# Performance work log

Measured on AMD Instinct MI355X. Metric: run time of the kernel, lower is better.

The kernel has to match this reference:

```python
import jax, jax.numpy as jnp
import numpy as np

N = 100000
E = 3200000
IN_DIM = 500
HID = 64
OUT_DIM = 40
K = 10
ALPHA = 0.1
BN_EPS = 1e-5


def setup_inputs() -> dict:
    key = jax.random.key(0)
    ks = jax.random.split(key, 10)
    x = jax.random.normal(ks[0], (N, IN_DIM), dtype=jnp.float32)
    edge_index = jax.random.randint(ks[1], (2, E), 0, N, dtype=jnp.int64)
    W1 = jax.random.normal(ks[2], (IN_DIM, HID), dtype=jnp.float32) / np.sqrt(IN_DIM)
    b1 = jnp.zeros((HID,), dtype=jnp.float32)
    bn_gamma = jnp.ones((HID,), dtype=jnp.float32)
    bn_beta = jnp.zeros((HID,), dtype=jnp.float32)
    bn_mean = jax.random.normal(ks[3], (HID,), dtype=jnp.float32) * 0.1
    bn_var = jax.random.uniform(ks[4], (HID,), dtype=jnp.float32) + 0.5
    W2 = jax.random.normal(ks[5], (HID, OUT_DIM), dtype=jnp.float32) / np.sqrt(HID)
    b2 = jnp.zeros((OUT_DIM,), dtype=jnp.float32)
    return {"x": x, "edge_index": edge_index, "W1": W1, "b1": b1,
            "bn_gamma": bn_gamma, "bn_beta": bn_beta, "bn_mean": bn_mean,
            "bn_var": bn_var, "W2": W2, "b2": b2}


def _gcn_norm(edge_index):
    # PyG gcn_norm with add_self_loops=True, symmetric normalization.
    row = jnp.concatenate([edge_index[0], jnp.arange(N, dtype=edge_index.dtype)])
    col = jnp.concatenate([edge_index[1], jnp.arange(N, dtype=edge_index.dtype)])
    deg = jax.ops.segment_sum(jnp.ones_like(col, dtype=jnp.float32), col, num_segments=N)
    dinv = jnp.where(deg > 0, jax.lax.rsqrt(deg), 0.0)
    norm = dinv[row] * dinv[col]  # [E+N]
    return row, col, norm


def _appnp(x, row, col, norm):
    h = x
    def step(xk, _):
        msg = norm[:, None] * xk[row]                       # [E+N, HID] gather
        agg = jax.ops.segment_sum(msg, col, num_segments=N)  # scatter-add
        return (1.0 - ALPHA) * agg + ALPHA * h, None
    xK, _ = jax.lax.scan(step, x, None, length=K)
    return xK


def reference(x, edge_index, W1, b1, bn_gamma, bn_beta, bn_mean, bn_var, W2, b2):
    row, col, norm = _gcn_norm(edge_index)
    h = x @ W1 + b1                                   # lin1
    h = _appnp(h, row, col, norm)                     # K-step APPNP
    h = (h - bn_mean) * jax.lax.rsqrt(bn_var + BN_EPS) * bn_gamma + bn_beta  # BN (eval)
    # dropout is identity in eval mode
    emb = h @ W2 + b2                                 # lin2
    out = jax.nn.log_softmax(emb, axis=1)
    return out, emb
```

## Files before the change

### kernel.cpp

```cpp
#include <hip/hip_runtime.h>
#include <math.h>

#define N_NODES 100000
#define N_EDGES 3200000
#define IN_DIM  500
#define HID     64
#define OUT_DIM 40
#define K_ITERS 10
#define ALPHA   0.1f
#define BN_EPS  1e-5f

#define WPAD 48
#define YD   40
#define YH   20
#define NBUCK 782
#define TILE_A 8192
#define APG 48
#define NQ 8
#define QSHIFT 14

__device__ __forceinline__ void unpack8(uint4 v, float f[8]) {
    f[0] = __uint_as_float(v.x << 16);
    f[1] = __uint_as_float(v.x & 0xffff0000u);
    f[2] = __uint_as_float(v.y << 16);
    f[3] = __uint_as_float(v.y & 0xffff0000u);
    f[4] = __uint_as_float(v.z << 16);
    f[5] = __uint_as_float(v.z & 0xffff0000u);
    f[6] = __uint_as_float(v.w << 16);
    f[7] = __uint_as_float(v.w & 0xffff0000u);
}
__device__ __forceinline__ unsigned pack2(float a, float b) {
    unsigned ua = __float_as_uint(a);
    unsigned ub = __float_as_uint(b);
    ua += ((ua >> 16) & 1u) + 0x7fffu;
    ub += ((ub >> 16) & 1u) + 0x7fffu;
    return (ua >> 16) | (ub & 0xffff0000u);
}
__device__ __forceinline__ float edge_w(unsigned e) {
    return __uint_as_float((e >> 17) << 16);
}
__device__ __forceinline__ void fma8(float acc[8], float wgt, const float f[8]) {
#pragma unroll
    for (int i = 0; i < 8; ++i) acc[i] = fmaf(wgt, f[i], acc[i]);
}


__global__ void zero_cnt_kernel(int* __restrict__ cntq) {
    int i = blockIdx.x * 256 + threadIdx.x;
    if (i < NQ * N_NODES) cntq[i] = 0;
}

__global__ void hist_kernel(const int* __restrict__ ei, int* __restrict__ cntq) {
    int e = blockIdx.x * 256 + threadIdx.x;
    if (e < N_EDGES) {
        int r = ei[e];
        int c = ei[N_EDGES + e];
        atomicAdd(&cntq[(r >> QSHIFT) * N_NODES + c], 1);
    }
}

__global__ void reduce_kernel(const int* __restrict__ cntq, int* __restrict__ psum) {
    __shared__ int s[256];
    int i = blockIdx.x * 256 + threadIdx.x;
    int v = 0;
    if (i < N_NODES) {
#pragma unroll
        for (int q = 0; q < NQ; ++q) v += cntq[q * N_NODES + i];
    }
    s[threadIdx.x] = v;
    __syncthreads();
    for (int off = 128; off > 0; off >>= 1) {
        if (threadIdx.x < (unsigned)off) s[threadIdx.x] += s[threadIdx.x + off];
        __syncthreads();
    }
    if (threadIdx.x == 0) psum[blockIdx.x] = s[0];
}

__global__ void scanp_kernel(const int* __restrict__ psum, int* __restrict__ pexcl,
                             int nparts) {
    __shared__ int s[512];
    int t = threadIdx.x;
    int v = (t < nparts) ? psum[t] : 0;
    s[t] = v;
    __syncthreads();
    for (int off = 1; off < 512; off <<= 1) {
        int tv = (t >= off) ? s[t - off] : 0;
        __syncthreads();
        s[t] += tv;
        __syncthreads();
    }
    if (t < nparts) pexcl[t] = s[t] - v;
}

__global__ void apply_kernel(const int* __restrict__ cntq, const int* __restrict__ pexcl,
                             int* __restrict__ rowptr, float* __restrict__ dinv) {
    __shared__ int s[256];
    int t = threadIdx.x;
    int i = blockIdx.x * 256 + t;
    int v = 0;
    if (i < N_NODES) {
#pragma unroll
        for (int q = 0; q < NQ; ++q) v += cntq[q * N_NODES + i];
    }
    s[t] = v;
    __syncthreads();
    for (int off = 1; off < 256; off <<= 1) {
        int tv = (t >= off) ? s[t - off] : 0;
        __syncthreads();
        s[t] += tv;
        __syncthreads();
    }
    if (i < N_NODES) {
        int excl = pexcl[blockIdx.x] + s[t] - v;
        rowptr[i] = excl;
        dinv[i] = rsqrtf((float)(v + 1));
        if (i == N_NODES - 1) rowptr[N_NODES] = excl + v;
    }
}


__global__ void bcur_init_kernel(const int* __restrict__ rowptr, int* __restrict__ bcursor) {
    int i = blockIdx.x * 256 + threadIdx.x;
    if (i < NBUCK) bcursor[i] = rowptr[i << 7];
}

__global__ __launch_bounds__(256) void bucketA_kernel(const int* __restrict__ ei,
                                                      int* __restrict__ bcursor,
                                                      unsigned* __restrict__ ebuf) {
    __shared__ int cnt[NBUCK];
    __shared__ int gbase[NBUCK];
    for (int i = threadIdx.x; i < NBUCK; i += 256) cnt[i] = 0;
    __syncthreads();
    const int e0 = blockIdx.x * TILE_A;
    const int e1 = (e0 + TILE_A < N_EDGES) ? e0 + TILE_A : N_EDGES;
    for (int e = e0 + threadIdx.x; e < e1; e += 256)
        atomicAdd(&cnt[ei[N_EDGES + e] >> 7], 1);
    __syncthreads();
    for (int i = threadIdx.x; i < NBUCK; i += 256) {
        int n = cnt[i];
        gbase[i] = (n > 0) ? atomicAdd(&bcursor[i], n) : 0;
        cnt[i] = 0;
    }
    __syncthreads();
    for (int e = e0 + threadIdx.x; e < e1; e += 256) {
        int r = ei[e];
        int c = ei[N_EDGES + e];
        int b = c >> 7;
        int rank = atomicAdd(&cnt[b], 1);
        ebuf[gbase[b] + rank] = (unsigned)r | ((unsigned)(c & 127) << 17);
    }
}

__global__ __launch_bounds__(256) void bucketB_kernel(const unsigned* __restrict__ ebuf,
                                                      const int* __restrict__ rowptr,
                                                      const int* __restrict__ cntq,
                                                      const float* __restrict__ dinv,
                                                      unsigned* __restrict__ ew) {
    __shared__ int lcur[NQ * 128];
    __shared__ float ldinv[128];
    const int base = blockIdx.x << 7;
    const int nn = (N_NODES - base < 128) ? (N_NODES - base) : 128;
    if (threadIdx.x < (unsigned)nn) {
        const int gi = base + threadIdx.x;
        int run = rowptr[gi];
#pragma unroll
        for (int q = 0; q < NQ; ++q) {
            lcur[q * 128 + threadIdx.x] = run;
            run += cntq[q * N_NODES + gi];
        }
        ldinv[threadIdx.x] = dinv[gi];
    }
    __syncthreads();
    const int s0 = rowptr[base];
    const int hi = (base + 128 < N_NODES) ? base + 128 : N_NODES;
    const int s1 = rowptr[hi];
    for (int p = s0 + threadIdx.x; p < s1; p += 256) {
        unsigned v = ebuf[p];
        int r = v & 0x1ffff;
        int cl = v >> 17;
        int q = r >> QSHIFT;
        int pos = atomicAdd(&lcur[q * 128 + cl], 1);
        float w = dinv[r] * ldinv[cl];
        unsigned f = __float_as_uint(w) + 0x8000u;
        ew[pos] = (unsigned)r | ((f >> 16) << 17);
    }
}

__global__ void prep_kernel(const float* __restrict__ W2, const float* __restrict__ gamma,
                            const float* __restrict__ beta, const float* __restrict__ mean,
                            const float* __restrict__ var, const float* __restrict__ b1,
                            const float* __restrict__ b2, float* __restrict__ W2p,
                            float* __restrict__ c1, float* __restrict__ cbeta) {
    __shared__ float sc[64];
    __shared__ float sd[64];
    int t = threadIdx.x;
    if (t < 64) {
        float s = rsqrtf(var[t] + BN_EPS) * gamma[t];
        sc[t] = s;
        sd[t] = beta[t] - mean[t] * s;
    }
    __syncthreads();
    for (int i = t; i < 64 * OUT_DIM; i += 256) {
        int f = i / OUT_DIM;
        W2p[i] = sc[f] * W2[i];
    }
    if (t < WPAD) {
        if (t < OUT_DIM) {
            float acb = b2[t], ac1 = 0.f;
            for (int f = 0; f < 64; ++f) {
                float w2 = W2[f * OUT_DIM + t];
                acb = fmaf(sd[f], w2, acb);
                ac1 = fmaf(b1[f] * sc[f], w2, ac1);
            }
            cbeta[t] = acb;
            c1[t] = ac1;
        } else {
            c1[t] = 0.f;
        }
    }
}

__global__ __launch_bounds__(256) void wc_kernel(const float* __restrict__ W1,
                                                 const float* __restrict__ W2p,
                                                 float* __restrict__ Wc) {
    __shared__ float w2s[64 * OUT_DIM];
    for (int i = threadIdx.x; i < 64 * OUT_DIM; i += 256) w2s[i] = W2p[i];
    __syncthreads();
    int idx = blockIdx.x * 256 + threadIdx.x;
    if (idx >= IN_DIM * WPAD) return;
    int k = idx / WPAD, o = idx % WPAD;
    float a = 0.f;
    if (o < OUT_DIM) {
        const float* w1r = W1 + (size_t)k * HID;
#pragma unroll 8
        for (int f = 0; f < 64; ++f) a = fmaf(w1r[f], w2s[f * OUT_DIM + o], a);
    }
    Wc[idx] = a;
}

#define L1_M  128
#define L1_KC 20
#define L1_PITCH 132
__global__ __launch_bounds__(256) void lin1_kernel(const float* __restrict__ x,
                                                   const float* __restrict__ Wc,
                                                   const float* __restrict__ c1,
                                                   float* __restrict__ y0f,
                                                   unsigned* __restrict__ y0b) {
    __shared__ float xsT[L1_KC * L1_PITCH];
    __shared__ float wcs[L1_KC * WPAD];

    const int t = threadIdx.x;
    const int ng = t & 31;
    const int og = t >> 5;
    const int nbase = blockIdx.x * L1_M;

    const int srow = t >> 1;
    const int skb  = (t & 1) * 10;
    const int gsrc = nbase + srow;
    const int gcl  = (gsrc < N_NODES) ? gsrc : (N_NODES - 1);
    const float* xrow = x + (size_t)gcl * IN_DIM;

    float acc[4][6];
#pragma unroll
    for (int i = 0; i < 4; ++i)
#pragma unroll
        for (int j = 0; j < 6; ++j) acc[i][j] = 0.0f;

    float2 xr[5];
    float wr[4];
#pragma unroll
    for (int u = 0; u < 5; ++u) xr[u] = *(const float2*)(xrow + skb + 2 * u);
#pragma unroll
    for (int j = 0; j < 4; ++j) {
        int i = t + j * 256;
        if (i < L1_KC * WPAD) wr[j] = Wc[i];
    }

    for (int k0 = 0; k0 < IN_DIM; k0 += L1_KC) {
#pragma unroll
        for (int u = 0; u < 5; ++u) {
            xsT[(skb + 2 * u) * L1_PITCH + srow]     = xr[u].x;
            xsT[(skb + 2 * u + 1) * L1_PITCH + srow] = xr[u].y;
        }
#pragma unroll
        for (int j = 0; j < 4; ++j) {
            int i = t + j * 256;
            if (i < L1_KC * WPAD) wcs[i] = wr[j];
        }
        __syncthreads();

        const int kn = k0 + L1_KC;
        if (kn < IN_DIM) {
#pragma unroll
            for (int u = 0; u < 5; ++u) xr[u] = *(const float2*)(xrow + kn + skb + 2 * u);
#pragma unroll
            for (int j = 0; j < 4; ++j) {
                int i = t + j * 256;
                if (i < L1_KC * WPAD) wr[j] = Wc[(size_t)kn * WPAD + i];
            }
        }

#pragma unroll 4
        for (int k = 0; k < L1_KC; ++k) {
            const float4 xv = *(const float4*)&xsT[k * L1_PITCH + ng * 4];
            float w[6];
#pragma unroll
            for (int j = 0; j < 6; ++j) w[j] = wcs[k * WPAD + og * 6 + j];
            const float xr4[4] = {xv.x, xv.y, xv.z, xv.w};
#pragma unroll
            for (int i = 0; i < 4; ++i)
#pragma unroll
                for (int j = 0; j < 6; ++j)
                    acc[i][j] = fmaf(xr4[i], w[j], acc[i][j]);
        }
        __syncthreads();
    }

    float cc[6];
#pragma unroll
    for (int j = 0; j < 6; ++j) cc[j] = c1[og * 6 + j];
#pragma unroll
    for (int i = 0; i < 4; ++i) {
        const int n = nbase + ng * 4 + i;
        if (n < N_NODES) {
            float o[6];
#pragma unroll
            for (int j = 0; j < 6; ++j) o[j] = acc[i][j] + cc[j];
            float* yf = y0f + (size_t)n * YD + og * 6;
            unsigned* yb = y0b + (size_t)n * YH + og * 3;
            if (og < 6) {
                *(float2*)(yf)     = make_float2(o[0], o[1]);
                *(float2*)(yf + 2) = make_float2(o[2], o[3]);
                *(float2*)(yf + 4) = make_float2(o[4], o[5]);
                yb[0] = pack2(o[0], o[1]);
                yb[1] = pack2(o[2], o[3]);
                yb[2] = pack2(o[4], o[5]);
            } else if (og == 6) {
                *(float2*)(yf)     = make_float2(o[0], o[1]);
                *(float2*)(yf + 2) = make_float2(o[2], o[3]);
                yb[0] = pack2(o[0], o[1]);
                yb[1] = pack2(o[2], o[3]);
            }
        }
    }
}

template <bool LAST>
__global__ __launch_bounds__(256) void appnp40_kernel(const int* __restrict__ rowptr,
                                                      const unsigned* __restrict__ ew,
                                                      const float* __restrict__ dinv,
                                                      const unsigned* __restrict__ yin,
                                                      const float* __restrict__ h,
                                                      unsigned* __restrict__ yout,
                                                      float* __restrict__ yKf) {
    const int wv   = threadIdx.x >> 6;
    const int lane = threadIdx.x & 63;
    const int sub  = lane / 5;
    const int dl   = lane - sub * 5;
    const int node = blockIdx.x * APG + wv * 12 + sub;
    const bool act = (lane < 60) && (node < N_NODES);
    const int dl4  = dl * 4;

    int beg = 0, end = 0;
    float selfw = 0.f;
    if (act) {
        beg = rowptr[node];
        end = rowptr[node + 1];
        const float di = dinv[node];
        selfw = di * di;
    }

    uint4 vs = make_uint4(0, 0, 0, 0);
    float4 h0 = make_float4(0.f, 0.f, 0.f, 0.f), h1 = h0;
    if (act) {
        vs = *(const uint4*)(yin + (size_t)node * YH + dl4);
        h0 = *(const float4*)(h + (size_t)node * YD + dl * 8);
        h1 = *(const float4*)(h + (size_t)node * YD + dl * 8 + 4);
    }

    float acc[8];
#pragma unroll
    for (int i = 0; i < 8; ++i) acc[i] = 0.f;

    int p = beg;
    for (; p + 3 < end; p += 4) {
        const unsigned e0 = ew[p], e1 = ew[p + 1], e2 = ew[p + 2], e3 = ew[p + 3];
        const uint4 v0 = *(const uint4*)(yin + (size_t)(e0 & 0x1ffff) * YH + dl4);
        const uint4 v1 = *(const uint4*)(yin + (size_t)(e1 & 0x1ffff) * YH + dl4);
        const uint4 v2 = *(const uint4*)(yin + (size_t)(e2 & 0x1ffff) * YH + dl4);
        const uint4 v3 = *(const uint4*)(yin + (size_t)(e3 & 0x1ffff) * YH + dl4);
        float f[8];
        unpack8(v0, f); fma8(acc, edge_w(e0), f);
        unpack8(v1, f); fma8(acc, edge_w(e1), f);
        unpack8(v2, f); fma8(acc, edge_w(e2), f);
        unpack8(v3, f); fma8(acc, edge_w(e3), f);
    }
    for (; p < end; ++p) {
        const unsigned e0 = ew[p];
        const uint4 v0 = *(const uint4*)(yin + (size_t)(e0 & 0x1ffff) * YH + dl4);
        float f[8];
        unpack8(v0, f);
        fma8(acc, edge_w(e0), f);
    }

    if (act) {
        float fs[8];
        unpack8(vs, fs);
        const float ha[8] = {h0.x, h0.y, h0.z, h0.w, h1.x, h1.y, h1.z, h1.w};
        float o[8];
#pragma unroll
        for (int i = 0; i < 8; ++i)
            o[i] = (1.0f - ALPHA) * fmaf(selfw, fs[i], acc[i]) + ALPHA * ha[i];
        if (LAST) {
            *(float4*)(yKf + (size_t)node * YD + dl * 8)     = make_float4(o[0], o[1], o[2], o[3]);
            *(float4*)(yKf + (size_t)node * YD + dl * 8 + 4) = make_float4(o[4], o[5], o[6], o[7]);
        } else {
            uint4 w;
            w.x = pack2(o[0], o[1]);
            w.y = pack2(o[2], o[3]);
            w.z = pack2(o[4], o[5]);
            w.w = pack2(o[6], o[7]);
            *(uint4*)(yout + (size_t)node * YH + dl4) = w;
        }
    }
}

__global__ __launch_bounds__(256) void final_kernel(const float* __restrict__ yKf,
                                                    const float* __restrict__ cbeta,
                                                    float* __restrict__ out_ls,
                                                    float* __restrict__ out_emb) {
    const int lane = threadIdx.x & 63;
    const int wv   = threadIdx.x >> 6;
    const int node = blockIdx.x * 4 + wv;

    float e = 0.0f;
    if (lane < OUT_DIM) e = yKf[(size_t)node * YD + lane] + cbeta[lane];
    float ev = (lane < OUT_DIM) ? e : -INFINITY;
    float m = ev;
#pragma unroll
    for (int off = 32; off > 0; off >>= 1) m = fmaxf(m, __shfl_xor(m, off, 64));
    float p = (lane < OUT_DIM) ? expf(ev - m) : 0.0f;
    float s = p;
#pragma unroll
    for (int off = 32; off > 0; off >>= 1) s += __shfl_xor(s, off, 64);
    if (lane < OUT_DIM) {
        float ls = ev - m - logf(s);
        out_ls[(size_t)node * OUT_DIM + lane] = ls;
        out_emb[(size_t)node * OUT_DIM + lane] = e;
    }
}


extern "C" void kernel_launch(void* const* d_in, const int* in_sizes, int n_in,
                              void* d_out, int out_size, void* d_ws, size_t ws_size,
                              hipStream_t stream) {
    const float* x     = (const float*)d_in[0];
    const int*   ei    = (const int*)d_in[1];
    const float* W1    = (const float*)d_in[2];
    const float* b1    = (const float*)d_in[3];
    const float* gamma = (const float*)d_in[4];
    const float* beta  = (const float*)d_in[5];
    const float* mean  = (const float*)d_in[6];
    const float* var   = (const float*)d_in[7];
    const float* W2    = (const float*)d_in[8];
    const float* b2    = (const float*)d_in[9];

    char* ws = (char*)d_ws;
    size_t off = 0;
    auto alloc = [&](size_t bytes) { char* p = ws + off; off += (bytes + 255) & ~(size_t)255; return p; };

    unsigned* ew     = (unsigned*)alloc((size_t)N_EDGES * 4);
    unsigned* ebuf   = (unsigned*)alloc((size_t)N_EDGES * 4);
    float*    y0f    = (float*)   alloc((size_t)N_NODES * YD * 4);
    float*    yKf    = (float*)   alloc((size_t)N_NODES * YD * 4);
    unsigned* y0b    = (unsigned*)alloc((size_t)N_NODES * YH * 4);
    unsigned* ya     = (unsigned*)alloc((size_t)N_NODES * YH * 4);
    unsigned* yb     = (unsigned*)alloc((size_t)N_NODES * YH * 4);
    float*    Wc     = (float*)   alloc((size_t)IN_DIM * WPAD * 4);
    float*    W2p    = (float*)   alloc(64 * OUT_DIM * 4);
    float*    c1     = (float*)   alloc(WPAD * 4);
    float*    cbeta  = (float*)   alloc(OUT_DIM * 4);
    int*      cntq   = (int*)     alloc((size_t)NQ * N_NODES * 4);
    float*    dinv   = (float*)   alloc(N_NODES * 4);
    int*      rowptr = (int*)     alloc((N_NODES + 1) * 4);
    int*      bcursor= (int*)     alloc(NBUCK * 4);
    int*      psum   = (int*)     alloc(1600 * 4);
    int*      pexcl  = (int*)     alloc(1600 * 4);

    float* out_ls  = (float*)d_out;
    float* out_emb = (float*)d_out + (size_t)N_NODES * OUT_DIM;

    const int NB_N = (N_NODES + 255) / 256;
    const int NB_E = (N_EDGES + 255) / 256;
    const int NB_A = (N_EDGES + TILE_A - 1) / TILE_A;
    const int NB_P = (N_NODES + APG - 1) / APG;
    const int NB_Z = (NQ * N_NODES + 255) / 256;

    zero_cnt_kernel<<<NB_Z, 256, 0, stream>>>(cntq);
    hist_kernel<<<NB_E, 256, 0, stream>>>(ei, cntq);
    reduce_kernel<<<NB_N, 256, 0, stream>>>(cntq, psum);
    scanp_kernel<<<1, 512, 0, stream>>>(psum, pexcl, NB_N);
    apply_kernel<<<NB_N, 256, 0, stream>>>(cntq, pexcl, rowptr, dinv);
    bcur_init_kernel<<<(NBUCK + 255) / 256, 256, 0, stream>>>(rowptr, bcursor);
    bucketA_kernel<<<NB_A, 256, 0, stream>>>(ei, bcursor, ebuf);
    bucketB_kernel<<<NBUCK, 256, 0, stream>>>(ebuf, rowptr, cntq, dinv, ew);

    prep_kernel<<<1, 256, 0, stream>>>(W2, gamma, beta, mean, var, b1, b2, W2p, c1, cbeta);
    wc_kernel<<<(IN_DIM * WPAD + 255) / 256, 256, 0, stream>>>(W1, W2p, Wc);
    lin1_kernel<<<(N_NODES + L1_M - 1) / L1_M, 256, 0, stream>>>(x, Wc, c1, y0f, y0b);

    const unsigned* cur = y0b;
    unsigned* nxt = ya;
    unsigned* buf[2] = {ya, yb};
    for (int k = 0; k < K_ITERS - 1; ++k) {
        appnp40_kernel<false><<<NB_P, 256, 0, stream>>>(rowptr, ew, dinv, cur,
                                                        y0f, nxt, nullptr);
        cur = nxt;
        nxt = buf[(k + 1) & 1];
    }
    appnp40_kernel<true><<<NB_P, 256, 0, stream>>>(rowptr, ew, dinv, cur,
                                                   y0f, nullptr, yKf);

    final_kernel<<<N_NODES / 4, 256, 0, stream>>>(yKf, cbeta, out_ls, out_emb);
}
```

Before: 1.171 ms.

## Sort nodes by degree for APPNP, add nontemporal gathers, shrink lin1 tile

Adds a counting sort of nodes by in-degree (histogram, scan, permutation kernels) so each APPNP wave processes nodes of similar degree, in descending order, which reduces lane divergence and load imbalance in the gather loop. Neighbor feature gathers now use nontemporal loads. The lin1 GEMM tile is halved from 128 to 64 rows per block, so only half the threads stage x. The changes add four small launches and an indirection through perm, and the nontemporal hint may lower cache reuse of the 4 MB feature table.

```diff
diff --git a/kernel.cpp b/kernel.cpp
--- a/kernel.cpp
+++ b/kernel.cpp
@@ -18,6 +18,9 @@
 #define APG 48
 #define NQ 8
 #define QSHIFT 14
+#define DMAX 512
+
+typedef unsigned uv4 __attribute__((ext_vector_type(4)));
 
 __device__ __forceinline__ void unpack8(uint4 v, float f[8]) {
     f[0] = __uint_as_float(v.x << 16);
@@ -43,6 +46,10 @@
 #pragma unroll
     for (int i = 0; i < 8; ++i) acc[i] = fmaf(wgt, f[i], acc[i]);
 }
+__device__ __forceinline__ uint4 ldnt4(const unsigned* p) {
+    uv4 v = __builtin_nontemporal_load((const uv4*)p);
+    return make_uint4(v.x, v.y, v.z, v.w);
+}
 
 
 __global__ void zero_cnt_kernel(int* __restrict__ cntq) {
@@ -115,6 +122,53 @@
         rowptr[i] = excl;
         dinv[i] = rsqrtf((float)(v + 1));
         if (i == N_NODES - 1) rowptr[N_NODES] = excl + v;
+    }
+}
+
+
+__global__ void zero_dc_kernel(int* __restrict__ dcnt) {
+    int i = blockIdx.x * 256 + threadIdx.x;
+    if (i < DMAX) dcnt[i] = 0;
+}
+
+__global__ void dhist_kernel(const int* __restrict__ rowptr, int* __restrict__ dcnt) {
+    __shared__ int s[DMAX];
+    for (int i = threadIdx.x; i < DMAX; i += 256) s[i] = 0;
+    __syncthreads();
+    int i = blockIdx.x * 256 + threadIdx.x;
+    if (i < N_NODES) {
+        int d = rowptr[i + 1] - rowptr[i];
+        if (d > DMAX - 1) d = DMAX - 1;
+        atomicAdd(&s[d], 1);
+    }
+    __syncthreads();
+    for (int i = threadIdx.x; i < DMAX; i += 256)
+        if (s[i]) atomicAdd(&dcnt[i], s[i]);
+}
+
+__global__ void dscan_kernel(const int* __restrict__ dcnt, int* __restrict__ doff) {
+    __shared__ int s[DMAX];
+    int t = threadIdx.x;
+    int v = dcnt[t];
+    s[t] = v;
+    __syncthreads();
+    for (int off = 1; off < DMAX; off <<= 1) {
+        int tv = (t >= off) ? s[t - off] : 0;
+        __syncthreads();
+        s[t] += tv;
+        __syncthreads();
+    }
+    doff[t] = s[t] - v;
+}
+
+__global__ void dperm_kernel(const int* __restrict__ rowptr, int* __restrict__ doff,
+                             int* __restrict__ perm) {
+    int i = blockIdx.x * 256 + threadIdx.x;
+    if (i < N_NODES) {
+        int d = rowptr[i + 1] - rowptr[i];
+        if (d > DMAX - 1) d = DMAX - 1;
+        int pos = atomicAdd(&doff[d], 1);
+        perm[N_NODES - 1 - pos] = i;
     }
 }
 
@@ -238,9 +292,9 @@
     Wc[idx] = a;
 }
 
-#define L1_M  128
+#define L1_M  64
 #define L1_KC 20
-#define L1_PITCH 132
+#define L1_PITCH 66
 __global__ __launch_bounds__(256) void lin1_kernel(const float* __restrict__ x,
                                                    const float* __restrict__ Wc,
                                                    const float* __restrict__ c1,
@@ -254,22 +308,25 @@
     const int og = t >> 5;
     const int nbase = blockIdx.x * L1_M;
 
+    const bool stager = (t < 128);
     const int srow = t >> 1;
     const int skb  = (t & 1) * 10;
     const int gsrc = nbase + srow;
     const int gcl  = (gsrc < N_NODES) ? gsrc : (N_NODES - 1);
     const float* xrow = x + (size_t)gcl * IN_DIM;
 
-    float acc[4][6];
-#pragma unroll
-    for (int i = 0; i < 4; ++i)
+    float acc[2][6];
+#pragma unroll
+    for (int i = 0; i < 2; ++i)
 #pragma unroll
         for (int j = 0; j < 6; ++j) acc[i][j] = 0.0f;
 
     float2 xr[5];
     float wr[4];
-#pragma unroll
-    for (int u = 0; u < 5; ++u) xr[u] = *(const float2*)(xrow + skb + 2 * u);
+    if (stager) {
+#pragma unroll
+        for (int u = 0; u < 5; ++u) xr[u] = *(const float2*)(xrow + skb + 2 * u);
+    }
 #pragma unroll
     for (int j = 0; j < 4; ++j) {
         int i = t + j * 256;
@@ -277,10 +334,12 @@
     }
 
     for (int k0 = 0; k0 < IN_DIM; k0 += L1_KC) {
-#pragma unroll
-        for (int u = 0; u < 5; ++u) {
-            xsT[(skb + 2 * u) * L1_PITCH + srow]     = xr[u].x;
-            xsT[(skb + 2 * u + 1) * L1_PITCH + srow] = xr[u].y;
+        if (stager) {
+#pragma unroll
+            for (int u = 0; u < 5; ++u) {
+                xsT[(skb + 2 * u) * L1_PITCH + srow]     = xr[u].x;
+                xsT[(skb + 2 * u + 1) * L1_PITCH + srow] = xr[u].y;
+            }
         }
 #pragma unroll
         for (int j = 0; j < 4; ++j) {
@@ -291,8 +350,10 @@
 
         const int kn = k0 + L1_KC;
         if (kn < IN_DIM) {
-#pragma unroll
-            for (int u = 0; u < 5; ++u) xr[u] = *(const float2*)(xrow + kn + skb + 2 * u);
+            if (stager) {
+#pragma unroll
+                for (int u = 0; u < 5; ++u) xr[u] = *(const float2*)(xrow + kn + skb + 2 * u);
+            }
 #pragma unroll
             for (int j = 0; j < 4; ++j) {
                 int i = t + j * 256;
@@ -302,16 +363,16 @@
 
 #pragma unroll 4
         for (int k = 0; k < L1_KC; ++k) {
-            const float4 xv = *(const float4*)&xsT[k * L1_PITCH + ng * 4];
+            const float2 xv = *(const float2*)&xsT[k * L1_PITCH + ng * 2];
             float w[6];
 #pragma unroll
             for (int j = 0; j < 6; ++j) w[j] = wcs[k * WPAD + og * 6 + j];
-            const float xr4[4] = {xv.x, xv.y, xv.z, xv.w};
-#pragma unroll
-            for (int i = 0; i < 4; ++i)
+            const float xr2[2] = {xv.x, xv.y};
+#pragma unroll
+            for (int i = 0; i < 2; ++i)
 #pragma unroll
                 for (int j = 0; j < 6; ++j)
-                    acc[i][j] = fmaf(xr4[i], w[j], acc[i][j]);
+                    acc[i][j] = fmaf(xr2[i], w[j], acc[i][j]);
         }
         __syncthreads();
     }
@@ -320,8 +381,8 @@
 #pragma unroll
     for (int j = 0; j < 6; ++j) cc[j] = c1[og * 6 + j];
 #pragma unroll
-    for (int i = 0; i < 4; ++i) {
-        const int n = nbase + ng * 4 + i;
+    for (int i = 0; i < 2; ++i) {
+        const int n = nbase + ng * 2 + i;
         if (n < N_NODES) {
             float o[6];
 #pragma unroll
@@ -349,6 +410,7 @@
 __global__ __launch_bounds__(256) void appnp40_kernel(const int* __restrict__ rowptr,
                                                       const unsigned* __restrict__ ew,
                                                       const float* __restrict__ dinv,
+                                                      const int* __restrict__ perm,
                                                       const unsigned* __restrict__ yin,
                                                       const float* __restrict__ h,
                                                       unsigned* __restrict__ yout,
@@ -357,8 +419,9 @@
     const int lane = threadIdx.x & 63;
     const int sub  = lane / 5;
     const int dl   = lane - sub * 5;
-    const int node = blockIdx.x * APG + wv * 12 + sub;
-    const bool act = (lane < 60) && (node < N_NODES);
+    const int slot = blockIdx.x * APG + wv * 12 + sub;
+    const bool act = (lane < 60) && (slot < N_NODES);
+    const int node = act ? perm[slot] : 0;
     const int dl4  = dl * 4;
 
     int beg = 0, end = 0;
@@ -385,10 +448,10 @@
     int p = beg;
     for (; p + 3 < end; p += 4) {
         const unsigned e0 = ew[p], e1 = ew[p + 1], e2 = ew[p + 2], e3 = ew[p + 3];
-        const uint4 v0 = *(const uint4*)(yin + (size_t)(e0 & 0x1ffff) * YH + dl4);
-        const uint4 v1 = *(const uint4*)(yin + (size_t)(e1 & 0x1ffff) * YH + dl4);
-        const uint4 v2 = *(const uint4*)(yin + (size_t)(e2 & 0x1ffff) * YH + dl4);
-        const uint4 v3 = *(const uint4*)(yin + (size_t)(e3 & 0x1ffff) * YH + dl4);
+        const uint4 v0 = ldnt4(yin + (size_t)(e0 & 0x1ffff) * YH + dl4);
+        const uint4 v1 = ldnt4(yin + (size_t)(e1 & 0x1ffff) * YH + dl4);
+        const uint4 v2 = ldnt4(yin + (size_t)(e2 & 0x1ffff) * YH + dl4);
+        const uint4 v3 = ldnt4(yin + (size_t)(e3 & 0x1ffff) * YH + dl4);
         float f[8];
         unpack8(v0, f); fma8(acc, edge_w(e0), f);
         unpack8(v1, f); fma8(acc, edge_w(e1), f);
@@ -397,7 +460,7 @@
     }
     for (; p < end; ++p) {
         const unsigned e0 = ew[p];
-        const uint4 v0 = *(const uint4*)(yin + (size_t)(e0 & 0x1ffff) * YH + dl4);
+        const uint4 v0 = ldnt4(yin + (size_t)(e0 & 0x1ffff) * YH + dl4);
         float f[8];
         unpack8(v0, f);
         fma8(acc, edge_w(e0), f);
@@ -483,9 +546,12 @@
     int*      cntq   = (int*)     alloc((size_t)NQ * N_NODES * 4);
     float*    dinv   = (float*)   alloc(N_NODES * 4);
     int*      rowptr = (int*)     alloc((N_NODES + 1) * 4);
+    int*      perm   = (int*)     alloc(N_NODES * 4);
     int*      bcursor= (int*)     alloc(NBUCK * 4);
     int*      psum   = (int*)     alloc(1600 * 4);
     int*      pexcl  = (int*)     alloc(1600 * 4);
+    int*      dcnt   = (int*)     alloc(DMAX * 4);
+    int*      doff   = (int*)     alloc(DMAX * 4);
 
     float* out_ls  = (float*)d_out;
     float* out_emb = (float*)d_out + (size_t)N_NODES * OUT_DIM;
@@ -501,6 +567,12 @@
     reduce_kernel<<<NB_N, 256, 0, stream>>>(cntq, psum);
     scanp_kernel<<<1, 512, 0, stream>>>(psum, pexcl, NB_N);
     apply_kernel<<<NB_N, 256, 0, stream>>>(cntq, pexcl, rowptr, dinv);
+
+    zero_dc_kernel<<<2, 256, 0, stream>>>(dcnt);
+    dhist_kernel<<<NB_N, 256, 0, stream>>>(rowptr, dcnt);
+    dscan_kernel<<<1, DMAX, 0, stream>>>(dcnt, doff);
+    dperm_kernel<<<NB_N, 256, 0, stream>>>(rowptr, doff, perm);
+
     bcur_init_kernel<<<(NBUCK + 255) / 256, 256, 0, stream>>>(rowptr, bcursor);
     bucketA_kernel<<<NB_A, 256, 0, stream>>>(ei, bcursor, ebuf);
     bucketB_kernel<<<NBUCK, 256, 0, stream>>>(ebuf, rowptr, cntq, dinv, ew);
@@ -513,12 +585,12 @@
     unsigned* nxt = ya;
     unsigned* buf[2] = {ya, yb};
     for (int k = 0; k < K_ITERS - 1; ++k) {
-        appnp40_kernel<false><<<NB_P, 256, 0, stream>>>(rowptr, ew, dinv, cur,
+        appnp40_kernel<false><<<NB_P, 256, 0, stream>>>(rowptr, ew, dinv, perm, cur,
                                                         y0f, nxt, nullptr);
         cur = nxt;
         nxt = buf[(k + 1) & 1];
     }
-    appnp40_kernel<true><<<NB_P, 256, 0, stream>>>(rowptr, ew, dinv, cur,
+    appnp40_kernel<true><<<NB_P, 256, 0, stream>>>(rowptr, ew, dinv, perm, cur,
                                                    y0f, nullptr, yKf);
 
     final_kernel<<<N_NODES / 4, 256, 0, stream>>>(yKf, cbeta, out_ls, out_emb);
```

Result: slower. 1.739 ms (+48.6%).

## Pad bf16 rows, use sc0 inline-asm gathers, shrink lin1 tile

Applied to the files above, without the earlier changes.

Pads the bf16 propagation rows from 20 to 24 dwords so each row starts on a 32-byte boundary. The neighbour gathers become inline-asm global_load_dwordx4 with the sc0 cache modifier and an explicit wait after each batch of four, aiming to change how gathered rows are cached. The lin1 tile is halved to 64 rows per block, which gives more blocks but uses only half the threads to stage x. The padding enlarges the gathered array, and the explicit s_waitcnt may stop the compiler from overlapping these loads with other work.

```diff
diff --git a/kernel.cpp b/kernel.cpp
--- a/kernel.cpp
+++ b/kernel.cpp
@@ -12,14 +12,16 @@
 
 #define WPAD 48
 #define YD   40
-#define YH   20
+#define YH   24
 #define NBUCK 782
 #define TILE_A 8192
 #define APG 48
 #define NQ 8
 #define QSHIFT 14
 
-__device__ __forceinline__ void unpack8(uint4 v, float f[8]) {
+typedef unsigned uv4 __attribute__((ext_vector_type(4)));
+
+__device__ __forceinline__ void unpack8(uv4 v, float f[8]) {
     f[0] = __uint_as_float(v.x << 16);
     f[1] = __uint_as_float(v.x & 0xffff0000u);
     f[2] = __uint_as_float(v.y << 16);
@@ -42,6 +44,28 @@
 __device__ __forceinline__ void fma8(float acc[8], float wgt, const float f[8]) {
 #pragma unroll
     for (int i = 0; i < 8; ++i) acc[i] = fmaf(wgt, f[i], acc[i]);
+}
+
+__device__ __forceinline__ void gather4_sc0(const unsigned* p0, const unsigned* p1,
+                                            const unsigned* p2, const unsigned* p3,
+                                            uv4& v0, uv4& v1, uv4& v2, uv4& v3) {
+    asm volatile(
+        "global_load_dwordx4 %0, %4, off sc0\n\t"
+        "global_load_dwordx4 %1, %5, off sc0\n\t"
+        "global_load_dwordx4 %2, %6, off sc0\n\t"
+        "global_load_dwordx4 %3, %7, off sc0\n\t"
+        "s_waitcnt vmcnt(0)"
+        : "=&v"(v0), "=&v"(v1), "=&v"(v2), "=&v"(v3)
+        : "v"(p0), "v"(p1), "v"(p2), "v"(p3)
+        : "memory");
+}
+__device__ __forceinline__ uv4 gather1_sc0(const unsigned* p) {
+    uv4 v;
+    asm volatile(
+        "global_load_dwordx4 %0, %1, off sc0\n\t"
+        "s_waitcnt vmcnt(0)"
+        : "=&v"(v) : "v"(p) : "memory");
+    return v;
 }
 
 
@@ -238,9 +262,9 @@
     Wc[idx] = a;
 }
 
-#define L1_M  128
+#define L1_M  64
 #define L1_KC 20
-#define L1_PITCH 132
+#define L1_PITCH 66
 __global__ __launch_bounds__(256) void lin1_kernel(const float* __restrict__ x,
                                                    const float* __restrict__ Wc,
                                                    const float* __restrict__ c1,
@@ -254,22 +278,25 @@
     const int og = t >> 5;
     const int nbase = blockIdx.x * L1_M;
 
+    const bool stager = (t < 128);
     const int srow = t >> 1;
     const int skb  = (t & 1) * 10;
     const int gsrc = nbase + srow;
     const int gcl  = (gsrc < N_NODES) ? gsrc : (N_NODES - 1);
     const float* xrow = x + (size_t)gcl * IN_DIM;
 
-    float acc[4][6];
-#pragma unroll
-    for (int i = 0; i < 4; ++i)
+    float acc[2][6];
+#pragma unroll
+    for (int i = 0; i < 2; ++i)
 #pragma unroll
         for (int j = 0; j < 6; ++j) acc[i][j] = 0.0f;
 
     float2 xr[5];
     float wr[4];
-#pragma unroll
-    for (int u = 0; u < 5; ++u) xr[u] = *(const float2*)(xrow + skb + 2 * u);
+    if (stager) {
+#pragma unroll
+        for (int u = 0; u < 5; ++u) xr[u] = *(const float2*)(xrow + skb + 2 * u);
+    }
 #pragma unroll
     for (int j = 0; j < 4; ++j) {
         int i = t + j * 256;
@@ -277,10 +304,12 @@
     }
 
     for (int k0 = 0; k0 < IN_DIM; k0 += L1_KC) {
-#pragma unroll
-        for (int u = 0; u < 5; ++u) {
-            xsT[(skb + 2 * u) * L1_PITCH + srow]     = xr[u].x;
-            xsT[(skb + 2 * u + 1) * L1_PITCH + srow] = xr[u].y;
+        if (stager) {
+#pragma unroll
+            for (int u = 0; u < 5; ++u) {
+                xsT[(skb + 2 * u) * L1_PITCH + srow]     = xr[u].x;
+                xsT[(skb + 2 * u + 1) * L1_PITCH + srow] = xr[u].y;
+            }
         }
 #pragma unroll
         for (int j = 0; j < 4; ++j) {
@@ -291,8 +320,10 @@
 
         const int kn = k0 + L1_KC;
         if (kn < IN_DIM) {
-#pragma unroll
-            for (int u = 0; u < 5; ++u) xr[u] = *(const float2*)(xrow + kn + skb + 2 * u);
+            if (stager) {
+#pragma unroll
+                for (int u = 0; u < 5; ++u) xr[u] = *(const float2*)(xrow + kn + skb + 2 * u);
+            }
 #pragma unroll
             for (int j = 0; j < 4; ++j) {
                 int i = t + j * 256;
@@ -302,16 +333,16 @@
 
 #pragma unroll 4
         for (int k = 0; k < L1_KC; ++k) {
-            const float4 xv = *(const float4*)&xsT[k * L1_PITCH + ng * 4];
+            const float2 xv = *(const float2*)&xsT[k * L1_PITCH + ng * 2];
             float w[6];
 #pragma unroll
             for (int j = 0; j < 6; ++j) w[j] = wcs[k * WPAD + og * 6 + j];
-            const float xr4[4] = {xv.x, xv.y, xv.z, xv.w};
-#pragma unroll
-            for (int i = 0; i < 4; ++i)
+            const float xr2[2] = {xv.x, xv.y};
+#pragma unroll
+            for (int i = 0; i < 2; ++i)
 #pragma unroll
                 for (int j = 0; j < 6; ++j)
-                    acc[i][j] = fmaf(xr4[i], w[j], acc[i][j]);
+                    acc[i][j] = fmaf(xr2[i], w[j], acc[i][j]);
         }
         __syncthreads();
     }
@@ -320,8 +351,8 @@
 #pragma unroll
     for (int j = 0; j < 6; ++j) cc[j] = c1[og * 6 + j];
 #pragma unroll
-    for (int i = 0; i < 4; ++i) {
-        const int n = nbase + ng * 4 + i;
+    for (int i = 0; i < 2; ++i) {
+        const int n = nbase + ng * 2 + i;
         if (n < N_NODES) {
             float o[6];
 #pragma unroll
@@ -370,10 +401,10 @@
         selfw = di * di;
     }
 
-    uint4 vs = make_uint4(0, 0, 0, 0);
+    uv4 vs = {0, 0, 0, 0};
     float4 h0 = make_float4(0.f, 0.f, 0.f, 0.f), h1 = h0;
     if (act) {
-        vs = *(const uint4*)(yin + (size_t)node * YH + dl4);
+        vs = *(const uv4*)(yin + (size_t)node * YH + dl4);
         h0 = *(const float4*)(h + (size_t)node * YD + dl * 8);
         h1 = *(const float4*)(h + (size_t)node * YD + dl * 8 + 4);
     }
@@ -385,10 +416,12 @@
     int p = beg;
     for (; p + 3 < end; p += 4) {
         const unsigned e0 = ew[p], e1 = ew[p + 1], e2 = ew[p + 2], e3 = ew[p + 3];
-        const uint4 v0 = *(const uint4*)(yin + (size_t)(e0 & 0x1ffff) * YH + dl4);
-        const uint4 v1 = *(const uint4*)(yin + (size_t)(e1 & 0x1ffff) * YH + dl4);
-        const uint4 v2 = *(const uint4*)(yin + (size_t)(e2 & 0x1ffff) * YH + dl4);
-        const uint4 v3 = *(const uint4*)(yin + (size_t)(e3 & 0x1ffff) * YH + dl4);
+        const unsigned* p0 = yin + (size_t)(e0 & 0x1ffff) * YH + dl4;
+        const unsigned* p1 = yin + (size_t)(e1 & 0x1ffff) * YH + dl4;
+        const unsigned* p2 = yin + (size_t)(e2 & 0x1ffff) * YH + dl4;
+        const unsigned* p3 = yin + (size_t)(e3 & 0x1ffff) * YH + dl4;
+        uv4 v0, v1, v2, v3;
+        gather4_sc0(p0, p1, p2, p3, v0, v1, v2, v3);
         float f[8];
         unpack8(v0, f); fma8(acc, edge_w(e0), f);
         unpack8(v1, f); fma8(acc, edge_w(e1), f);
@@ -397,7 +430,7 @@
     }
     for (; p < end; ++p) {
         const unsigned e0 = ew[p];
-        const uint4 v0 = *(const uint4*)(yin + (size_t)(e0 & 0x1ffff) * YH + dl4);
+        const uv4 v0 = gather1_sc0(yin + (size_t)(e0 & 0x1ffff) * YH + dl4);
         float f[8];
         unpack8(v0, f);
         fma8(acc, edge_w(e0), f);
```

Measured after the change: 1.266 ms. 8.1% more time.
